# Kernel optimization log

Measured on AMD Instinct MI355X. Metric: run time of the kernel, lower is better.

The kernel has to match this reference:

```python
import jax, jax.numpy as jnp
import numpy as np

HIDDEN = 1152
NUM_HEADS = 16
HEAD_DIM = HIDDEN // NUM_HEADS  # 72
SEQ = 4096


def rotate_half(x):
    x1 = x[..., : x.shape[-1] // 2]
    x2 = x[..., x.shape[-1] // 2 :]
    return jnp.concatenate((-x2, x1), axis=-1)


def setup_inputs() -> dict:
    key = jax.random.key(0)
    ks = jax.random.split(key, 8)
    hidden_states = jax.random.normal(ks[0], (SEQ, HIDDEN), dtype=jnp.float32)
    cu_seqlens = jnp.sort(jax.random.randint(ks[1], (3,), 0, SEQ)).astype(jnp.int32)
    # rotary embeddings: realistic cos/sin tables
    pos = jnp.arange(SEQ, dtype=jnp.float32)[:, None]
    inv_freq = 1.0 / (10000.0 ** (jnp.arange(0, HEAD_DIM, 2, dtype=jnp.float32) / HEAD_DIM))
    freqs = pos * inv_freq[None, :]  # (SEQ, HEAD_DIM//2)
    emb = jnp.concatenate([freqs, freqs], axis=-1)  # (SEQ, HEAD_DIM)
    cos = jnp.cos(emb)
    sin = jnp.sin(emb)
    std = 0.02
    Wqkv = jax.random.normal(ks[2], (HIDDEN, 3 * HIDDEN), dtype=jnp.float32) * std
    bqkv = jnp.zeros((3 * HIDDEN,), dtype=jnp.float32)
    Wproj = jax.random.normal(ks[3], (HIDDEN, HIDDEN), dtype=jnp.float32) * std
    bproj = jnp.zeros((HIDDEN,), dtype=jnp.float32)
    return {
        "hidden_states": hidden_states,
        "cu_seqlens": cu_seqlens,
        "cos": cos,
        "sin": sin,
        "Wqkv": Wqkv,
        "bqkv": bqkv,
        "Wproj": Wproj,
        "bproj": bproj,
    }


def reference(hidden_states, cu_seqlens, cos, sin, Wqkv, bqkv, Wproj, bproj):
    seq_len = hidden_states.shape[0]
    scale = HEAD_DIM ** -0.5
    qkv = hidden_states @ Wqkv + bqkv  # (S, 3*H)
    qkv = qkv.reshape(seq_len, 3, NUM_HEADS, HEAD_DIM).transpose(1, 0, 2, 3)
    q, k, v = qkv[0], qkv[1], qkv[2]  # each (S, nH, hd)
    # inline RoPE in fp32
    orig_dtype = q.dtype
    qf = q.astype(jnp.float32)
    kf = k.astype(jnp.float32)
    c = cos[:, None, :].astype(jnp.float32)
    s = sin[:, None, :].astype(jnp.float32)
    q = (qf * c + rotate_half(qf) * s).astype(orig_dtype)
    k = (kf * c + rotate_half(kf) * s).astype(orig_dtype)
    # (nH, S, hd)
    q = q.transpose(1, 0, 2)
    k = k.transpose(1, 0, 2)
    v = v.transpose(1, 0, 2)
    attn = jnp.einsum('hqd,hkd->hqk', q, k) * scale
    attn = jax.nn.softmax(attn, axis=-1)
    out = jnp.einsum('hqk,hkd->hqd', attn, v)  # (nH, S, hd)
    out = out.transpose(1, 0, 2).reshape(seq_len, HIDDEN)
    return out @ Wproj + bproj
```

## Files before the change

kernel.cpp:

```cpp
#include <hip/hip_runtime.h>
#include <hip/hip_bf16.h>
#include <stdint.h>

#define SEQ 4096
#define HID 1152
#define NH  16
#define HD  72
#define N3  3456
#define DQ  80
#define QBLK 256
#define TILE_ELEMS 14336

typedef __bf16 bf16;
typedef __bf16 bf16x8 __attribute__((ext_vector_type(8)));
typedef float  f32x4  __attribute__((ext_vector_type(4)));
typedef float  f32x16 __attribute__((ext_vector_type(16)));
typedef uint32_t u32x4 __attribute__((ext_vector_type(4)));

#define EXP2F(x) __builtin_amdgcn_exp2f(x)
#define PLSWAP(a, b) asm("v_permlane32_swap_b32 %0, %1" : "+v"(a), "+v"(b))

__device__ __forceinline__ void gload_lds16(const void* g, void* l) {
    __builtin_amdgcn_global_load_lds(
        (__attribute__((address_space(1))) void*)(void*)g,
        (__attribute__((address_space(3))) void*)l, 16, 0, 0);
}
__device__ __forceinline__ uint16_t bfbits(float x) {
    return __builtin_bit_cast(uint16_t, (bf16)x);
}

__global__ __launch_bounds__(256)
void prep(const float* __restrict__ hidden, const float* __restrict__ Wqkv,
          const float* __restrict__ Wproj, bf16* __restrict__ hid_b,
          bf16* __restrict__ WqkvT, bf16* __restrict__ WprojT)
{
    __shared__ float tl[32][33];
    int b = blockIdx.x, tid = threadIdx.x;
    if (b < 2304) {
        int i = b * 256 + tid;
        const float4* p = (const float4*)hidden + (size_t)i * 2;
        float4 a = p[0], c = p[1];
        bf16x8 o;
        o[0]=(bf16)a.x; o[1]=(bf16)a.y; o[2]=(bf16)a.z; o[3]=(bf16)a.w;
        o[4]=(bf16)c.x; o[5]=(bf16)c.y; o[6]=(bf16)c.z; o[7]=(bf16)c.w;
        ((bf16x8*)hid_b)[i] = o;
        return;
    }
    const float* in; bf16* out; int R, C, c0, r0;
    if (b < 6192) {
        int bb = b - 2304;
        in = Wqkv; out = WqkvT; R = HID; C = N3;
        c0 = (bb % 108) * 32; r0 = (bb / 108) * 32;
    } else {
        int bb = b - 6192;
        in = Wproj; out = WprojT; R = HID; C = HID;
        c0 = (bb % 36) * 32; r0 = (bb / 36) * 32;
    }
    int tx = tid & 31, ty = tid >> 5;
#pragma unroll
    for (int i = 0; i < 4; ++i)
        tl[ty + 8*i][tx] = in[(size_t)(r0 + ty + 8*i) * C + c0 + tx];
    __syncthreads();
#pragma unroll
    for (int i = 0; i < 4; ++i)
        out[(size_t)(c0 + ty + 8*i) * R + r0 + tx] = (bf16)tl[tx][ty + 8*i];
}

template<int OUT_F32>
__global__ __launch_bounds__(256)
void gemm_bt(const bf16* __restrict__ A, const bf16* __restrict__ BT,
             const float* __restrict__ bias, void* __restrict__ out,
             int M, int N, int K)
{
    __shared__ __align__(16) bf16 As[128 * 64];
    __shared__ __align__(16) bf16 Bs[128 * 64];
    int tid = threadIdx.x;
    int lane = tid & 63, w = tid >> 6;
    int wm = w & 1, wn = w >> 1;
    int orig = blockIdx.y * gridDim.x + blockIdx.x;
    int xcd = orig & 7, v = orig >> 3;
    int mpx = gridDim.x >> 3;
    int m0 = (xcd * mpx + (v % mpx)) * 128;
    int n0 = (v / mpx) * 128;
    int lq = lane & 15, lk = lane >> 4;

    int kx0 = ((lk ^ (lq & 7)) << 4);
    int kx1 = (((4 + lk) ^ (lq & 7)) << 4);

    f32x4 acc[4][4] = {};

    for (int k0 = 0; k0 < K; k0 += 64) {
        __syncthreads();
#pragma unroll
        for (int j = 0; j < 4; ++j) {
            int c = j * 256 + tid;
            int row = c >> 3, kc = c & 7;
            int koff = k0 + ((kc ^ (row & 7)) << 3);
            gload_lds16(A  + (size_t)(m0 + row) * K + koff, (char*)As + c * 16);
            gload_lds16(BT + (size_t)(n0 + row) * K + koff, (char*)Bs + c * 16);
        }
        __syncthreads();
#pragma unroll
        for (int ks = 0; ks < 2; ++ks) {
            int kx = ks ? kx1 : kx0;
            bf16x8 af[4], bfr[4];
#pragma unroll
            for (int m = 0; m < 4; ++m)
                af[m] = *(const bf16x8*)((char*)As + (wm * 64 + m * 16 + lq) * 128 + kx);
#pragma unroll
            for (int n = 0; n < 4; ++n)
                bfr[n] = *(const bf16x8*)((char*)Bs + (wn * 64 + n * 16 + lq) * 128 + kx);
#pragma unroll
            for (int m = 0; m < 4; ++m)
#pragma unroll
                for (int n = 0; n < 4; ++n)
                    acc[m][n] = __builtin_amdgcn_mfma_f32_16x16x32_bf16(af[m], bfr[n], acc[m][n], 0, 0, 0);
        }
    }

    int rb = m0 + wm * 64, cb = n0 + wn * 64;
#pragma unroll
    for (int m = 0; m < 4; ++m) {
#pragma unroll
        for (int n = 0; n < 4; ++n) {
            int col = cb + n * 16 + lq;
            float b = bias[col];
#pragma unroll
            for (int r = 0; r < 4; ++r) {
                int row = rb + m * 16 + lk * 4 + r;
                float v2 = acc[m][n][r] + b;
                if (OUT_F32) ((float*)out)[(size_t)row * N + col] = v2;
                else         ((bf16*)out)[(size_t)row * N + col] = (bf16)v2;
            }
        }
    }
}

__global__ __launch_bounds__(256)
void pack(const bf16* __restrict__ qkv, const float* __restrict__ cs,
          const float* __restrict__ sn, bf16* __restrict__ Qp,
          bf16* __restrict__ KVp)
{
    __shared__ __align__(16) bf16 tl[64][80];
    int b = blockIdx.x, tid = threadIdx.x;
    if (b < 32768) {
        int idx = b * 256 + tid;
        int dd = idx & 127;
        int s  = (idx >> 7) & (SEQ - 1);
        int h  = idx >> 19;
        float qv = 0.f, kv = 0.f;
        if (dd < HD) {
            const bf16* row = qkv + (size_t)s * N3 + h * HD;
            float c  = cs[s * HD + dd], si = sn[s * HD + dd];
            int   dp = (dd < 36) ? dd + 36 : dd - 36;
            float sg = (dd < 36) ? -1.f : 1.f;
            float qa = (float)row[dd],       qb = (float)row[dp];
            float ka = (float)row[HID + dd], kb = (float)row[HID + dp];
            qv = (qa * c + sg * qb * si) * (0.11785113019775793f * 1.4426950408889634f);
            kv =  ka * c + sg * kb * si;
        }
        int t = s >> 6, key = s & 63;
        int chunk = key * 16 + ((dd >> 3) ^ (key & 15));
        KVp[((size_t)(h * 64 + t)) * TILE_ELEMS + chunk * 8 + (dd & 7)] = (bf16)kv;
        if (dd < DQ) Qp[((size_t)h * SEQ + s) * DQ + dd] = (bf16)qv;
        return;
    }
    int bb = b - 32768;
    int t = bb & 63, h = bb >> 6, s0 = t * 64;
    for (int i = tid; i < 64 * 9; i += 256) {
        int key = i / 9, c8 = (i % 9) * 8;
        *(bf16x8*)&tl[key][c8] =
            *(const bf16x8*)&qkv[(size_t)(s0 + key) * N3 + 2 * HID + h * HD + c8];
    }
    __syncthreads();
    bf16* dst = KVp + ((size_t)(h * 64 + t)) * TILE_ELEMS + 8192;
    for (int vcid = tid; vcid < 768; vcid += 256) {
        int d = vcid >> 3, cpos = vcid & 7;
        int kb8 = (cpos ^ (d & 7)) << 3;
        bf16x8 v;
#pragma unroll
        for (int j = 0; j < 8; ++j)
            v[j] = (d < HD) ? tl[kb8 + j][d] : ((d == HD) ? (bf16)1.f : (bf16)0.f);
        *(bf16x8*)&dst[vcid * 8] = v;
    }
}

__global__ __launch_bounds__(512, 2)
void attn_fwd11(const bf16* __restrict__ Qp, const bf16* __restrict__ KVp,
                bf16* __restrict__ Oout)
{
    __shared__ __align__(16) char smem[86016];

    const int o = blockIdx.x;
    const int x = o & 7, s = o >> 3;
    const int h  = x * 2 + (s >> 4);
    const int q0 = (s & 15) * QBLK;
    const int tid = threadIdx.x, lane = tid & 63, w = tid >> 6;
    const int ql = lane & 31, hi = lane >> 5;
    const int q  = q0 + w * 32 + ql;

    bf16x8 qf[5];
    const bf16* qbase = Qp + ((size_t)h * SEQ + q) * DQ + hi * 8;
#pragma unroll
    for (int ks = 0; ks < 5; ++ks) qf[ks] = *(const bf16x8*)(qbase + ks * 16);

    int aK[5], aV[4];
#pragma unroll
    for (int ks = 0; ks < 5; ++ks)
        aK[ks] = ql * 256 + (((ks * 2 + hi) ^ (ql & 15)) * 16);
#pragma unroll
    for (int u = 0; u < 4; ++u)
        aV[u] = 16384 + ql * 128 + (((u * 2 + hi) ^ (ql & 7)) * 16);

    f32x16 o_[3] = {};

    const bf16* kvbase = KVp + (size_t)h * (64 * TILE_ELEMS) + (size_t)tid * 8;

#define STAGE(T, DB) do {                                                      \
        const bf16* s_ = kvbase + (size_t)(T) * TILE_ELEMS;                    \
        char* d_ = smem + (DB) + tid * 16;                                     \
        _Pragma("unroll")                                                      \
        for (int j_ = 0; j_ < 3; ++j_)                                         \
            gload_lds16(s_ + j_ * 4096, d_ + j_ * 8192);                       \
        if (tid < 256) gload_lds16(s_ + 12288, d_ + 24576);                    \
    } while (0)

    auto qk = [&](const char* bK, f32x16& sa, f32x16& sb) {
        __builtin_amdgcn_s_setprio(1);
#pragma unroll
        for (int ks = 0; ks < 5; ++ks) {
            bf16x8 kf = *(const bf16x8*)(bK + aK[ks]);
            sa = __builtin_amdgcn_mfma_f32_32x32x16_bf16(kf, qf[ks], sa, 0, 0, 0);
        }
#pragma unroll
        for (int ks = 0; ks < 5; ++ks) {
            bf16x8 kf = *(const bf16x8*)(bK + 8192 + aK[ks]);
            sb = __builtin_amdgcn_mfma_f32_32x32x16_bf16(kf, qf[ks], sb, 0, 0, 0);
        }
        __builtin_amdgcn_s_setprio(0);
    };

    auto expv = [&](const f32x16& sa, const f32x16& sb, const char* bV) {
        uint32_t wd[16];
#pragma unroll
        for (int i = 0; i < 8; ++i) {
            wd[i]   = (uint32_t)bfbits(EXP2F(sa[2*i])) | ((uint32_t)bfbits(EXP2F(sa[2*i+1])) << 16);
            wd[8+i] = (uint32_t)bfbits(EXP2F(sb[2*i])) | ((uint32_t)bfbits(EXP2F(sb[2*i+1])) << 16);
        }
        PLSWAP(wd[0], wd[2]);   PLSWAP(wd[1], wd[3]);
        PLSWAP(wd[4], wd[6]);   PLSWAP(wd[5], wd[7]);
        PLSWAP(wd[8], wd[10]);  PLSWAP(wd[9], wd[11]);
        PLSWAP(wd[12], wd[14]); PLSWAP(wd[13], wd[15]);
        u32x4 u0 = {wd[0],wd[1],wd[2],wd[3]},   u1 = {wd[4],wd[5],wd[6],wd[7]};
        u32x4 u2 = {wd[8],wd[9],wd[10],wd[11]}, u3 = {wd[12],wd[13],wd[14],wd[15]};
        bf16x8 pb[4] = { __builtin_bit_cast(bf16x8, u0), __builtin_bit_cast(bf16x8, u1),
                         __builtin_bit_cast(bf16x8, u2), __builtin_bit_cast(bf16x8, u3) };
        __builtin_amdgcn_s_setprio(1);
#pragma unroll
        for (int db = 0; db < 3; ++db)
#pragma unroll
            for (int u = 0; u < 4; ++u) {
                bf16x8 vf = *(const bf16x8*)(bV + db * 4096 + aV[u]);
                o_[db] = __builtin_amdgcn_mfma_f32_32x32x16_bf16(vf, pb[u], o_[db], 0, 0, 0);
            }
        __builtin_amdgcn_s_setprio(0);
    };

    f32x16 pa = {}, pb_ = {};

    STAGE(0, 0);
    asm volatile("s_waitcnt vmcnt(0)" ::: "memory");
    __builtin_amdgcn_s_barrier();
    STAGE(1, 28672);
    qk(smem, pa, pb_);
    asm volatile("s_waitcnt vmcnt(0)" ::: "memory");
    __builtin_amdgcn_s_barrier();

#define BODY(T, KB, VB, SB) do {                                               \
        if ((T) < 63) STAGE((T) + 1, SB);                                      \
        f32x16 ca = {}, cb = {};                                               \
        qk(smem + (KB), ca, cb);                                               \
        expv(pa, pb_, smem + (VB));                                            \
        pa = ca; pb_ = cb;                                                     \
        __builtin_amdgcn_sched_barrier(0);                                     \
        asm volatile("s_waitcnt vmcnt(0)" ::: "memory");                       \
        __builtin_amdgcn_s_barrier();                                          \
    } while (0)

    for (int t = 1; t < 64; t += 3) {
        BODY(t,     28672, 0,     57344);
        BODY(t + 1, 57344, 28672, 0);
        BODY(t + 2, 0,     57344, 28672);
    }
    expv(pa, pb_, smem);
#undef BODY
#undef STAGE

    __syncthreads();
    bf16* Os = (bf16*)smem;
    {
        float lv  = o_[2][4];
        float lo_ = __shfl_xor(lv, 32);
        float invl = 1.0f / (hi ? lo_ : lv);
        int qloc = w * 32 + ql;
#pragma unroll
        for (int db = 0; db < 3; ++db)
#pragma unroll
            for (int r = 0; r < 16; ++r) {
                int dloc = (r & 3) + 8 * (r >> 2) + 4 * hi;
                int d = db * 32 + dloc;
                if (d < HD) Os[qloc * 82 + d] = (bf16)(o_[db][r] * invl);
            }
    }
    __syncthreads();
    for (int i = tid; i < QBLK * 36; i += 512) {
        int row = i / 36, c = i % 36;
        uint32_t val = *(const uint32_t*)((const char*)Os + row * 164 + c * 4);
        *(uint32_t*)((char*)Oout + (size_t)(q0 + row) * 2304 + h * 144 + c * 4) = val;
    }
}

extern "C" void kernel_launch(void* const* d_in, const int* in_sizes, int n_in,
                              void* d_out, int out_size, void* d_ws, size_t ws_size,
                              hipStream_t stream)
{
    const float* hidden = (const float*)d_in[0];
    const float* cosT  = (const float*)d_in[2];
    const float* sinT  = (const float*)d_in[3];
    const float* Wqkv  = (const float*)d_in[4];
    const float* bqkv  = (const float*)d_in[5];
    const float* Wproj = (const float*)d_in[6];
    const float* bproj = (const float*)d_in[7];

    char* ws = (char*)d_ws;
    size_t off = 0;
    auto alloc = [&](size_t bytes) {
        char* p = ws + off;
        off += (bytes + 255) & ~(size_t)255;
        return p;
    };
    bf16* hid_b  = (bf16*)alloc((size_t)SEQ * HID * 2);
    bf16* WqkvT  = (bf16*)alloc((size_t)N3  * HID * 2);
    bf16* WprojT = (bf16*)alloc((size_t)HID * HID * 2);
    bf16* qkv_b  = (bf16*)alloc((size_t)SEQ * N3  * 2);
    bf16* Qp     = (bf16*)alloc((size_t)NH * SEQ * DQ * 2);
    bf16* KVp    = (bf16*)alloc((size_t)NH * 64 * TILE_ELEMS * 2);
    bf16* attno  = hid_b;

    prep<<<7488, 256, 0, stream>>>(hidden, Wqkv, Wproj, hid_b, WqkvT, WprojT);
    gemm_bt<0><<<dim3(SEQ / 128, N3 / 128), 256, 0, stream>>>(hid_b, WqkvT, bqkv, qkv_b,
                                                              SEQ, N3, HID);
    pack<<<33792, 256, 0, stream>>>(qkv_b, cosT, sinT, Qp, KVp);
    attn_fwd11<<<dim3(SEQ / QBLK * NH), 512, 0, stream>>>(Qp, KVp, attno);
    gemm_bt<1><<<dim3(SEQ / 128, HID / 128), 256, 0, stream>>>(attno, WprojT, bproj, d_out,
                                                               SEQ, HID, HID);
}
```

Before: 201.7 us.

## Compact K/V tile layout to drop padding and shrink LDS footprint

Repacks the per-head K/V tiles so that K rows hold 80 elements instead of 128 and V holds only the 72 real dims plus a ones column, removing most of the zero padding. This cuts the global bytes staged per tile and reduces shared memory per block from about 84KB to 58KB. V reads for the padded third block are redirected to a zeroed LDS slot. In exchange the addressing becomes irregular: K uses only an 8-way swizzle, which may raise LDS bank conflicts, and the pack kernel uses div/mod by 80 and launches fewer blocks.

```diff
diff --git a/kernel.cpp b/kernel.cpp
--- a/kernel.cpp
+++ b/kernel.cpp
@@ -9,7 +9,10 @@
 #define N3  3456
 #define DQ  80
 #define QBLK 256
-#define TILE_ELEMS 14336
+#define TILE_B 19584
+#define TILE_E 9792
+#define VBASE 10240
+#define ZOFF  58752
 
 typedef __bf16 bf16;
 typedef __bf16 bf16x8 __attribute__((ext_vector_type(8)));
@@ -143,11 +146,11 @@
 {
     __shared__ __align__(16) bf16 tl[64][80];
     int b = blockIdx.x, tid = threadIdx.x;
-    if (b < 32768) {
+    if (b < 20480) {
         int idx = b * 256 + tid;
-        int dd = idx & 127;
-        int s  = (idx >> 7) & (SEQ - 1);
-        int h  = idx >> 19;
+        int dd = idx % 80;
+        int rest = idx / 80;
+        int s = rest & (SEQ - 1), h = rest >> 12;
         float qv = 0.f, kv = 0.f;
         if (dd < HD) {
             const bf16* row = qkv + (size_t)s * N3 + h * HD;
@@ -160,12 +163,13 @@
             kv =  ka * c + sg * kb * si;
         }
         int t = s >> 6, key = s & 63;
-        int chunk = key * 16 + ((dd >> 3) ^ (key & 15));
-        KVp[((size_t)(h * 64 + t)) * TILE_ELEMS + chunk * 8 + (dd & 7)] = (bf16)kv;
-        if (dd < DQ) Qp[((size_t)h * SEQ + s) * DQ + dd] = (bf16)qv;
+        int dchunk = dd >> 3;
+        int pos = (dchunk < 8) ? (dchunk ^ (key & 7)) : dchunk;
+        KVp[((size_t)(h * 64 + t)) * TILE_E + key * 80 + pos * 8 + (dd & 7)] = (bf16)kv;
+        Qp[((size_t)h * SEQ + s) * DQ + dd] = (bf16)qv;
         return;
     }
-    int bb = b - 32768;
+    int bb = b - 20480;
     int t = bb & 63, h = bb >> 6, s0 = t * 64;
     for (int i = tid; i < 64 * 9; i += 256) {
         int key = i / 9, c8 = (i % 9) * 8;
@@ -173,23 +177,23 @@
             *(const bf16x8*)&qkv[(size_t)(s0 + key) * N3 + 2 * HID + h * HD + c8];
     }
     __syncthreads();
-    bf16* dst = KVp + ((size_t)(h * 64 + t)) * TILE_ELEMS + 8192;
-    for (int vcid = tid; vcid < 768; vcid += 256) {
+    bf16* dst = KVp + ((size_t)(h * 64 + t)) * TILE_E + 5120;
+    for (int vcid = tid; vcid < 584; vcid += 256) {
         int d = vcid >> 3, cpos = vcid & 7;
         int kb8 = (cpos ^ (d & 7)) << 3;
         bf16x8 v;
 #pragma unroll
         for (int j = 0; j < 8; ++j)
-            v[j] = (d < HD) ? tl[kb8 + j][d] : ((d == HD) ? (bf16)1.f : (bf16)0.f);
+            v[j] = (d < HD) ? tl[kb8 + j][d] : (bf16)1.f;
         *(bf16x8*)&dst[vcid * 8] = v;
     }
 }
 
 __global__ __launch_bounds__(512, 2)
-void attn_fwd11(const bf16* __restrict__ Qp, const bf16* __restrict__ KVp,
+void attn_fwd13(const bf16* __restrict__ Qp, const bf16* __restrict__ KVp,
                 bf16* __restrict__ Oout)
 {
-    __shared__ __align__(16) char smem[86016];
+    __shared__ __align__(16) char smem[59392];
 
     const int o = blockIdx.x;
     const int x = o & 7, s = o >> 3;
@@ -204,25 +208,27 @@
 #pragma unroll
     for (int ks = 0; ks < 5; ++ks) qf[ks] = *(const bf16x8*)(qbase + ks * 16);
 
-    int aK[5], aV[4];
-#pragma unroll
-    for (int ks = 0; ks < 5; ++ks)
-        aK[ks] = ql * 256 + (((ks * 2 + hi) ^ (ql & 15)) * 16);
+    int aK[5];
+#pragma unroll
+    for (int ks = 0; ks < 4; ++ks)
+        aK[ks] = ql * 160 + (((ks * 2 + hi) ^ (ql & 7)) * 16);
+    aK[4] = ql * 160 + (8 + hi) * 16;
+    int aV[4];
 #pragma unroll
     for (int u = 0; u < 4; ++u)
-        aV[u] = 16384 + ql * 128 + (((u * 2 + hi) ^ (ql & 7)) * 16);
+        aV[u] = VBASE + ql * 128 + (((u * 2 + hi) ^ (ql & 7)) * 16);
 
     f32x16 o_[3] = {};
 
-    const bf16* kvbase = KVp + (size_t)h * (64 * TILE_ELEMS) + (size_t)tid * 8;
+    const bf16* kvh = KVp + (size_t)h * (64 * TILE_E);
 
 #define STAGE(T, DB) do {                                                      \
-        const bf16* s_ = kvbase + (size_t)(T) * TILE_ELEMS;                    \
-        char* d_ = smem + (DB) + tid * 16;                                     \
+        const bf16* s_ = kvh + (size_t)(T) * TILE_E;                           \
         _Pragma("unroll")                                                      \
-        for (int j_ = 0; j_ < 3; ++j_)                                         \
-            gload_lds16(s_ + j_ * 4096, d_ + j_ * 8192);                       \
-        if (tid < 256) gload_lds16(s_ + 12288, d_ + 24576);                    \
+        for (int j_ = 0; j_ < 3; ++j_) {                                       \
+            int c_ = j_ * 512 + tid;                                           \
+            if (c_ < 1224) gload_lds16(s_ + c_ * 8, smem + (DB) + c_ * 16);    \
+        }                                                                      \
     } while (0)
 
     auto qk = [&](const char* bK, f32x16& sa, f32x16& sb) {
@@ -234,7 +240,7 @@
         }
 #pragma unroll
         for (int ks = 0; ks < 5; ++ks) {
-            bf16x8 kf = *(const bf16x8*)(bK + 8192 + aK[ks]);
+            bf16x8 kf = *(const bf16x8*)(bK + 5120 + aK[ks]);
             sb = __builtin_amdgcn_mfma_f32_32x32x16_bf16(kf, qf[ks], sb, 0, 0, 0);
         }
         __builtin_amdgcn_s_setprio(0);
@@ -260,7 +266,11 @@
         for (int db = 0; db < 3; ++db)
 #pragma unroll
             for (int u = 0; u < 4; ++u) {
-                bf16x8 vf = *(const bf16x8*)(bV + db * 4096 + aV[u]);
+                const char* pv;
+                if (db < 2)          pv = bV + db * 4096 + aV[u];
+                else if (ql <= 8)    pv = bV + 8192 + aV[u];
+                else                 pv = smem + ZOFF;
+                bf16x8 vf = *(const bf16x8*)pv;
                 o_[db] = __builtin_amdgcn_mfma_f32_32x32x16_bf16(vf, pb[u], o_[db], 0, 0, 0);
             }
         __builtin_amdgcn_s_setprio(0);
@@ -268,10 +278,11 @@
 
     f32x16 pa = {}, pb_ = {};
 
+    if (tid < 4) ((float*)(smem + ZOFF))[tid] = 0.f;
     STAGE(0, 0);
-    asm volatile("s_waitcnt vmcnt(0)" ::: "memory");
+    asm volatile("s_waitcnt vmcnt(0) lgkmcnt(0)" ::: "memory");
     __builtin_amdgcn_s_barrier();
-    STAGE(1, 28672);
+    STAGE(1, TILE_B);
     qk(smem, pa, pb_);
     asm volatile("s_waitcnt vmcnt(0)" ::: "memory");
     __builtin_amdgcn_s_barrier();
@@ -288,9 +299,9 @@
     } while (0)
 
     for (int t = 1; t < 64; t += 3) {
-        BODY(t,     28672, 0,     57344);
-        BODY(t + 1, 57344, 28672, 0);
-        BODY(t + 2, 0,     57344, 28672);
+        BODY(t,     TILE_B,     0,          2 * TILE_B);
+        BODY(t + 1, 2 * TILE_B, TILE_B,     0);
+        BODY(t + 2, 0,          2 * TILE_B, TILE_B);
     }
     expv(pa, pb_, smem);
 #undef BODY
@@ -344,14 +355,14 @@
     bf16* WprojT = (bf16*)alloc((size_t)HID * HID * 2);
     bf16* qkv_b  = (bf16*)alloc((size_t)SEQ * N3  * 2);
     bf16* Qp     = (bf16*)alloc((size_t)NH * SEQ * DQ * 2);
-    bf16* KVp    = (bf16*)alloc((size_t)NH * 64 * TILE_ELEMS * 2);
+    bf16* KVp    = (bf16*)alloc((size_t)NH * 64 * TILE_E * 2);
     bf16* attno  = hid_b;
 
     prep<<<7488, 256, 0, stream>>>(hidden, Wqkv, Wproj, hid_b, WqkvT, WprojT);
     gemm_bt<0><<<dim3(SEQ / 128, N3 / 128), 256, 0, stream>>>(hid_b, WqkvT, bqkv, qkv_b,
                                                               SEQ, N3, HID);
-    pack<<<33792, 256, 0, stream>>>(qkv_b, cosT, sinT, Qp, KVp);
-    attn_fwd11<<<dim3(SEQ / QBLK * NH), 512, 0, stream>>>(Qp, KVp, attno);
+    pack<<<21504, 256, 0, stream>>>(qkv_b, cosT, sinT, Qp, KVp);
+    attn_fwd13<<<dim3(SEQ / QBLK * NH), 512, 0, stream>>>(Qp, KVp, attno);
     gemm_bt<1><<<dim3(SEQ / 128, HID / 128), 256, 0, stream>>>(attno, WprojT, bproj, d_out,
                                                                SEQ, HID, HID);
 }
```

After: 197.8 us. About the same (-1.9%).
